# Performance work log

Hardware: AMD Instinct MI355X
Metric: run time of the kernel (lower is better)

Reference implementation:

```python
import jax, jax.numpy as jnp
import numpy as np

B, S, E, H = 2, 2048, 1024, 16
D = E // H  # head_dim = 64
SCALE = 1.0 / np.sqrt(D)


def setup_inputs() -> dict:
    key = jax.random.key(0)
    ks = jax.random.split(key, 5)
    std = 0.02
    return {
        "x": jax.random.normal(ks[0], (B, S, E), dtype=jnp.float32),
        "wq": jax.random.normal(ks[1], (E, E), dtype=jnp.float32) * std,
        "wk": jax.random.normal(ks[2], (E, E), dtype=jnp.float32) * std,
        "wv": jax.random.normal(ks[3], (E, E), dtype=jnp.float32) * std,
        "wo": jax.random.normal(ks[4], (E, E), dtype=jnp.float32) * std,
    }


def reference(x, wq, wk, wv, wo):
    # Linear projections (torch Linear: y = x @ W.T); weights stored as [out, in]
    q = jnp.einsum('bse,fe->bsf', x, wq)
    k = jnp.einsum('bse,fe->bsf', x, wk)
    v = jnp.einsum('bse,fe->bsf', x, wv)
    # split heads -> [B, H, S, D]
    q = q.reshape(B, S, H, D).transpose(0, 2, 1, 3)
    k = k.reshape(B, S, H, D).transpose(0, 2, 1, 3)
    v = v.reshape(B, S, H, D).transpose(0, 2, 1, 3)
    # scaled dot-product scores [B, H, S, S]
    scores = jnp.einsum('bhqd,bhkd->bhqk', q, k) * SCALE
    # causal mask: -inf above diagonal
    causal = jnp.triu(jnp.full((S, S), -jnp.inf, dtype=scores.dtype), k=1)
    scores = scores + causal[None, None, :, :]
    attn = jax.nn.softmax(scores, axis=-1)
    # dropout p=0 -> identity
    out = jnp.einsum('bhqk,bhkd->bhqd', attn, v)
    out = out.transpose(0, 2, 1, 3).reshape(B, S, E)
    return jnp.einsum('bse,fe->bsf', out, wo)
```

## Files before the change

### kernel.cpp

```cpp
#include <hip/hip_runtime.h>
#include <hip/hip_bf16.h>

#define B_ 2
#define S_ 2048
#define E_ 1024
#define H_ 16
#define D_ 64
#define QKV_N 3072
#define C2_ 0.18033688011112042f

typedef __attribute__((ext_vector_type(8))) unsigned short ushort8_t;
typedef __attribute__((ext_vector_type(8))) short short8_t;
typedef __attribute__((ext_vector_type(4))) float f32x4;

__device__ __forceinline__ unsigned short f2b(float f) {
    union { float f; unsigned u; } x; x.f = f;
    unsigned r = x.u + 0x7FFFu + ((x.u >> 16) & 1u);
    return (unsigned short)(r >> 16);
}
__device__ __forceinline__ ushort2 pkbf(float a, float b) {
    union { __hip_bfloat162 h; ushort2 u; } c;
    c.h = __float22bfloat162_rn(make_float2(a, b));
    return c.u;
}
__device__ __forceinline__ void glds16(const unsigned short* g, unsigned short* l) {
    __builtin_amdgcn_global_load_lds((const __attribute__((address_space(1))) void*)g,
                                     (__attribute__((address_space(3))) void*)l, 16, 0, 0);
}

__global__ __launch_bounds__(256) void cast_all(const float* __restrict__ x,
                                                const float* __restrict__ wq,
                                                const float* __restrict__ wk,
                                                const float* __restrict__ wv,
                                                const float* __restrict__ wo,
                                                unsigned short* __restrict__ xb,
                                                unsigned short* __restrict__ wb) {
    int idx = blockIdx.x * 256 + threadIdx.x;
    const float* src; unsigned short* dst; float s = 1.f; int j;
    if (idx < 1048576) {
        src = x; dst = xb; j = idx;
    } else {
        j = idx - 1048576;
        int y = j >> 18;
        src = (y == 0) ? wq : (y == 1) ? wk : (y == 2) ? wv : wo;
        dst = wb + (size_t)y * 1048576;
        j &= 262143;
        if (y == 0) s = C2_;
    }
    float4 v = ((const float4*)src)[j];
    ushort2 lo = pkbf(v.x * s, v.y * s), hi = pkbf(v.z * s, v.w * s);
    ((ushort4*)dst)[j] = make_ushort4(lo.x, lo.y, hi.x, hi.y);
}

template <int TM, bool OUT_BF16>
__device__ __forceinline__ void gemm_bt_body(const unsigned short* __restrict__ A,
                                             const unsigned short* __restrict__ Bt,
                                             void* __restrict__ Cout,
                                             int m0, int n0, int N, int K) {
    __shared__ unsigned short As[2 * TM * 32];
    __shared__ unsigned short Bs[2 * 128 * 32];
    const int tid = threadIdx.x;
    const int wave = tid >> 6;
    const int lane = tid & 63;
    const int wm = (wave >> 1) * (TM / 2);
    const int wn = (wave & 1) * 64;
    const int quad = lane >> 4;
    const int l15 = lane & 15;
    constexpr int MI = TM / 32;

    f32x4 acc[MI][4] = {};

    const int srow = lane >> 2;
    const int scb  = (lane & 3) * 8;
    const unsigned short* gB0 = Bt + (size_t)(n0 + wave * 32 + srow) * K + scb;
    const unsigned short* gB1 = gB0 + (size_t)16 * K;
    unsigned short* lB0 = Bs + wave * 1024;
    unsigned short* lB1 = lB0 + 512;
    const unsigned short* gA0;
    const unsigned short* gA1 = nullptr;
    unsigned short* lA0;
    unsigned short* lA1 = nullptr;
    if (TM == 128) {
        gA0 = A + (size_t)(m0 + wave * 32 + srow) * K + scb;
        gA1 = gA0 + (size_t)16 * K;
        lA0 = As + wave * 1024; lA1 = lA0 + 512;
    } else {
        gA0 = A + (size_t)(m0 + wave * 16 + srow) * K + scb;
        lA0 = As + wave * 512;
    }

    for (int k0 = 0; k0 < K; k0 += 64) {
        __syncthreads();
        glds16(gA0 + k0, lA0);
        glds16(gA0 + k0 + 32, lA0 + TM * 32);
        if (TM == 128) {
            glds16(gA1 + k0, lA1);
            glds16(gA1 + k0 + 32, lA1 + TM * 32);
        }
        glds16(gB0 + k0, lB0);
        glds16(gB0 + k0 + 32, lB0 + 128 * 32);
        glds16(gB1 + k0, lB1);
        glds16(gB1 + k0 + 32, lB1 + 128 * 32);
        __syncthreads();

#pragma unroll
        for (int h = 0; h < 2; ++h) {
            const unsigned short* ah = As + h * TM * 32;
            const unsigned short* bh = Bs + h * 128 * 32;
            short8_t af[MI], bfv[4];
#pragma unroll
            for (int mi = 0; mi < MI; ++mi)
                af[mi] = *(const short8_t*)(&ah[(wm + mi * 16 + l15) * 32 + quad * 8]);
#pragma unroll
            for (int ni = 0; ni < 4; ++ni)
                bfv[ni] = *(const short8_t*)(&bh[(wn + ni * 16 + l15) * 32 + quad * 8]);
#pragma unroll
            for (int mi = 0; mi < MI; ++mi)
#pragma unroll
                for (int ni = 0; ni < 4; ++ni)
                    acc[mi][ni] = __builtin_amdgcn_mfma_f32_16x16x32_bf16(
                        af[mi], bfv[ni], acc[mi][ni], 0, 0, 0);
        }
    }

#pragma unroll
    for (int mi = 0; mi < MI; ++mi)
#pragma unroll
        for (int ni = 0; ni < 4; ++ni)
#pragma unroll
            for (int r = 0; r < 4; ++r) {
                int row = m0 + wm + mi * 16 + quad * 4 + r;
                int col = n0 + wn + ni * 16 + l15;
                float val = acc[mi][ni][r];
                if (OUT_BF16)
                    ((unsigned short*)Cout)[(size_t)row * N + col] = f2b(val);
                else
                    ((float*)Cout)[(size_t)row * N + col] = val;
            }
}

__global__ __launch_bounds__(256, 3) void gemm_qkv(const unsigned short* __restrict__ xb,
                                                   const unsigned short* __restrict__ wqkv,
                                                   unsigned short* __restrict__ qkv) {
    int id = blockIdx.x + 24 * blockIdx.y;
    int sw = (id & 7) * 96 + (id >> 3);
    int n0 = (sw % 24) * 128;
    int m0 = (sw / 24) * 128;
    gemm_bt_body<128, true>(xb, wqkv, qkv, m0, n0, QKV_N, E_);
}

__global__ __launch_bounds__(256, 2) void gemm_out(const unsigned short* __restrict__ a,
                                                   const unsigned short* __restrict__ wob,
                                                   float* __restrict__ c) {
    gemm_bt_body<64, false>(a, wob, c, blockIdx.y * 64, blockIdx.x * 128, E_, E_);
}

__global__ __launch_bounds__(256) void transpose_v(const unsigned short* __restrict__ qkv,
                                                   unsigned short* __restrict__ Vt) {
    __shared__ unsigned short T[64][72];
    const int b = blockIdx.z, h = blockIdx.y, kt = blockIdx.x * 64;
    const int r = threadIdx.x >> 2;
    const int g = (threadIdx.x & 3) * 16;
    const size_t goff = (size_t)(b * S_ + kt + r) * QKV_N + 2048 + h * D_ + g;
    ushort8_t v0 = *(const ushort8_t*)(qkv + goff);
    ushort8_t v1 = *(const ushort8_t*)(qkv + goff + 8);
    *(ushort8_t*)(&T[r][g])     = v0;
    *(ushort8_t*)(&T[r][g + 8]) = v1;
    __syncthreads();
    ushort8_t o0, o1;
#pragma unroll
    for (int i = 0; i < 8; ++i) { o0[i] = T[g + i][r]; o1[i] = T[g + 8 + i][r]; }
    unsigned short* op = Vt + ((size_t)((b * H_ + h) * D_ + r)) * S_ + kt + g;
    *(ushort8_t*)(op)     = o0;
    *(ushort8_t*)(op + 8) = o1;
}

__global__ __launch_bounds__(512, 4) void attn_kernel(const unsigned short* __restrict__ QKV,
                                                      const unsigned short* __restrict__ Vtg,
                                                      unsigned short* __restrict__ O) {
    __shared__ unsigned short Ks[2][64 * 64];
    __shared__ unsigned short Vs[2][64 * 64];
    __shared__ unsigned short Ps[8][16 * 64];

    const int b = blockIdx.z, h = blockIdx.y;
    const int c = blockIdx.x;
    const int jp = (b == 0) ? c : (15 - c);
    const int tid = threadIdx.x;
    const int w = tid >> 6, lane = tid & 63;
    const int quad = lane >> 4, l15 = lane & 15;
    const int lx = l15 & 7;
    const int chunk = 2 * jp + ((w < 4) ? 1 : 0);
    const int Q0 = chunk * 64 + (w & 3) * 16;

    const size_t qo = (size_t)(b * S_ + Q0 + l15) * QKV_N + h * D_;
    short8_t bq0 = *(const short8_t*)(QKV + qo + quad * 8);
    short8_t bq1 = *(const short8_t*)(QKV + qo + 32 + quad * 8);

    f32x4 Oacc[4] = {};
    float lsum = 0.f;
    const int qg = Q0 + l15;

    const int fo0 = ((quad) ^ lx) * 8;
    const int fo1 = ((4 + quad) ^ lx) * 8;
    const int krow = l15 * 64;
    int pwo[4];
#pragma unroll
    for (int tm = 0; tm < 4; ++tm)
        pwo[tm] = ((tm * 2 + (quad >> 1)) ^ lx) * 8 + (quad & 1) * 4;

    const int srow = tid >> 3;
    const int scb  = tid & 7;
    const int swz  = (scb ^ (srow & 7)) * 8;
    const unsigned short* Kbase = QKV + (size_t)(b * S_) * QKV_N + 1024 + h * D_;
    const unsigned short* Vbase = Vtg + (size_t)((b * H_ + h) * D_) * S_;

    const int nT = jp + 1;
    for (int t = 0; t < nT; ++t) {
        const int kt0 = t * 128;
        ushort8_t ka = *(const ushort8_t*)(Kbase + (size_t)(kt0 + srow) * QKV_N + scb * 8);
        ushort8_t kb = *(const ushort8_t*)(Kbase + (size_t)(kt0 + 64 + srow) * QKV_N + scb * 8);
        ushort8_t va = *(const ushort8_t*)(Vbase + (size_t)srow * S_ + kt0 + scb * 8);
        ushort8_t vb = *(const ushort8_t*)(Vbase + (size_t)srow * S_ + kt0 + 64 + scb * 8);
        __syncthreads();
        *(ushort8_t*)(&Ks[0][srow * 64 + swz]) = ka;
        *(ushort8_t*)(&Ks[1][srow * 64 + swz]) = kb;
        *(ushort8_t*)(&Vs[0][srow * 64 + swz]) = va;
        *(ushort8_t*)(&Vs[1][srow * 64 + swz]) = vb;
        __syncthreads();

#pragma unroll
        for (int s = 0; s < 2; ++s) {
            const int kt = kt0 + s * 64;
            if (kt > Q0 + 15) continue;
            const bool h2 = (kt + 32 <= Q0 + 15);

            if (kt + 63 <= Q0) {
#pragma unroll
                for (int tm = 0; tm < 4; ++tm) {
                    short8_t ak0 = *(const short8_t*)(&Ks[s][tm * 1024 + krow + fo0]);
                    short8_t ak1 = *(const short8_t*)(&Ks[s][tm * 1024 + krow + fo1]);
                    f32x4 st = {0.f, 0.f, 0.f, 0.f};
                    st = __builtin_amdgcn_mfma_f32_16x16x32_bf16(ak0, bq0, st, 0, 0, 0);
                    st = __builtin_amdgcn_mfma_f32_16x16x32_bf16(ak1, bq1, st, 0, 0, 0);
                    float p0 = exp2f(st[0]), p1 = exp2f(st[1]);
                    float p2 = exp2f(st[2]), p3 = exp2f(st[3]);
                    lsum += (p0 + p1) + (p2 + p3);
                    ushort2 a = pkbf(p0, p1), c2 = pkbf(p2, p3);
                    *(ushort4*)(&Ps[w][krow + pwo[tm]]) = make_ushort4(a.x, a.y, c2.x, c2.y);
                }
            } else {
                const int need = h2 ? 4 : 2;
                for (int tm = 0; tm < need; ++tm) {
                    if (kt + tm * 16 <= Q0 + 15) {
                        short8_t ak0 = *(const short8_t*)(&Ks[s][tm * 1024 + krow + fo0]);
                        short8_t ak1 = *(const short8_t*)(&Ks[s][tm * 1024 + krow + fo1]);
                        f32x4 st = {0.f, 0.f, 0.f, 0.f};
                        st = __builtin_amdgcn_mfma_f32_16x16x32_bf16(ak0, bq0, st, 0, 0, 0);
                        st = __builtin_amdgcn_mfma_f32_16x16x32_bf16(ak1, bq1, st, 0, 0, 0);
                        const int kvb = kt + tm * 16 + quad * 4;
                        float p0 = (kvb     > qg) ? 0.f : exp2f(st[0]);
                        float p1 = (kvb + 1 > qg) ? 0.f : exp2f(st[1]);
                        float p2 = (kvb + 2 > qg) ? 0.f : exp2f(st[2]);
                        float p3 = (kvb + 3 > qg) ? 0.f : exp2f(st[3]);
                        lsum += (p0 + p1) + (p2 + p3);
                        ushort2 a = pkbf(p0, p1), c2 = pkbf(p2, p3);
                        *(ushort4*)(&Ps[w][krow + pwo[tm]]) = make_ushort4(a.x, a.y, c2.x, c2.y);
                    } else {
                        *(ushort4*)(&Ps[w][krow + pwo[tm]]) = make_ushort4(0, 0, 0, 0);
                    }
                }
            }

#pragma unroll
            for (int kh = 0; kh < 2; ++kh) {
                if (kh == 1 && !h2) break;
                const int fo = kh ? fo1 : fo0;
                short8_t bv[4];
#pragma unroll
                for (int tn = 0; tn < 4; ++tn)
                    bv[tn] = *(const short8_t*)(&Vs[s][tn * 1024 + krow + fo]);
                short8_t ap = *(const short8_t*)(&Ps[w][krow + fo]);
#pragma unroll
                for (int tn = 0; tn < 4; ++tn)
                    Oacc[tn] = __builtin_amdgcn_mfma_f32_16x16x32_bf16(
                        ap, bv[tn], Oacc[tn], 0, 0, 0);
            }
        }
    }

    float l = lsum;
    l += __shfl_xor(l, 16);
    l += __shfl_xor(l, 32);
    float inv = 1.f / l;
    float lir[4];
#pragma unroll
    for (int r = 0; r < 4; ++r)
        lir[r] = __shfl(inv, quad * 4 + r);
#pragma unroll
    for (int tn = 0; tn < 4; ++tn)
#pragma unroll
        for (int r = 0; r < 4; ++r) {
            int row = Q0 + quad * 4 + r;
            O[(size_t)(b * S_ + row) * E_ + h * D_ + tn * 16 + l15] =
                f2b(Oacc[tn][r] * lir[r]);
        }
}

extern "C" void kernel_launch(void* const* d_in, const int* in_sizes, int n_in,
                              void* d_out, int out_size, void* d_ws, size_t ws_size,
                              hipStream_t stream) {
    const float* x  = (const float*)d_in[0];
    const float* wq = (const float*)d_in[1];
    const float* wk = (const float*)d_in[2];
    const float* wv = (const float*)d_in[3];
    const float* wo = (const float*)d_in[4];
    float* out = (float*)d_out;

    unsigned short* ws   = (unsigned short*)d_ws;
    unsigned short* xb   = ws;
    unsigned short* wqkv = ws + 4194304;
    unsigned short* wob  = ws + 7340032;
    unsigned short* qkvb = ws + 8388608;
    unsigned short* ab   = ws + 20971520;
    unsigned short* vt   = xb;

    cast_all<<<8192, 256, 0, stream>>>(x, wq, wk, wv, wo, xb, wqkv);
    gemm_qkv<<<dim3(24, 32), 256, 0, stream>>>(xb, wqkv, qkvb);
    transpose_v<<<dim3(32, 16, 2), 256, 0, stream>>>(qkvb, vt);
    attn_kernel<<<dim3(16, 16, 2), 512, 0, stream>>>(qkvb, vt, ab);
    gemm_out<<<dim3(8, 64), 256, 0, stream>>>(ab, wob, out);
}
```

Baseline: 178.9 us.

## Fuse V transpose into QKV GEMM epilogue and rebalance causal chunk pairing

The QKV GEMM epilogue now writes V tiles transposed, packed into the V columns of the qkv buffer (two rows per head-dim channel). The attention kernel reads V^T directly from there, so the separate transpose_v launch and its extra global read/write pass go away. Attention work is also redistributed: each block now pairs query chunk c with chunk 31-c instead of the previous jp-based pairing. The trade-off is a more complex scattered epilogue store with 4-element ushort4 writes, and indexing that depends on the in-place layout being correct.

Measured after the change: 176.1 us. About the same (-1.6%).

```diff
diff --git a/kernel.cpp b/kernel.cpp
--- a/kernel.cpp
+++ b/kernel.cpp
@@ -52,7 +52,7 @@
     ((ushort4*)dst)[j] = make_ushort4(lo.x, lo.y, hi.x, hi.y);
 }
 
-template <int TM, bool OUT_BF16>
+template <int TM, bool OUT_BF16, bool VT>
 __device__ __forceinline__ void gemm_bt_body(const unsigned short* __restrict__ A,
                                              const unsigned short* __restrict__ Bt,
                                              void* __restrict__ Cout,
@@ -123,6 +123,22 @@
         }
     }
 
+    if (VT && n0 >= 2048) {
+#pragma unroll
+        for (int mi = 0; mi < MI; ++mi)
+#pragma unroll
+            for (int ni = 0; ni < 4; ++ni) {
+                int col = n0 + wn + ni * 16 + l15;
+                int r0  = m0 + wm + mi * 16 + quad * 4;
+                int bb  = r0 >> 11, s = r0 & 2047;
+                size_t drow = (size_t)bb * 2048 + 2 * (col - 2048) + (s >> 10);
+                unsigned short* dp = (unsigned short*)Cout + drow * QKV_N + 2048 + (s & 1023);
+                *(ushort4*)dp = make_ushort4(f2b(acc[mi][ni][0]), f2b(acc[mi][ni][1]),
+                                             f2b(acc[mi][ni][2]), f2b(acc[mi][ni][3]));
+            }
+        return;
+    }
+
 #pragma unroll
     for (int mi = 0; mi < MI; ++mi)
 #pragma unroll
@@ -146,37 +162,16 @@
     int sw = (id & 7) * 96 + (id >> 3);
     int n0 = (sw % 24) * 128;
     int m0 = (sw / 24) * 128;
-    gemm_bt_body<128, true>(xb, wqkv, qkv, m0, n0, QKV_N, E_);
+    gemm_bt_body<128, true, true>(xb, wqkv, qkv, m0, n0, QKV_N, E_);
 }
 
 __global__ __launch_bounds__(256, 2) void gemm_out(const unsigned short* __restrict__ a,
                                                    const unsigned short* __restrict__ wob,
                                                    float* __restrict__ c) {
-    gemm_bt_body<64, false>(a, wob, c, blockIdx.y * 64, blockIdx.x * 128, E_, E_);
-}
-
-__global__ __launch_bounds__(256) void transpose_v(const unsigned short* __restrict__ qkv,
-                                                   unsigned short* __restrict__ Vt) {
-    __shared__ unsigned short T[64][72];
-    const int b = blockIdx.z, h = blockIdx.y, kt = blockIdx.x * 64;
-    const int r = threadIdx.x >> 2;
-    const int g = (threadIdx.x & 3) * 16;
-    const size_t goff = (size_t)(b * S_ + kt + r) * QKV_N + 2048 + h * D_ + g;
-    ushort8_t v0 = *(const ushort8_t*)(qkv + goff);
-    ushort8_t v1 = *(const ushort8_t*)(qkv + goff + 8);
-    *(ushort8_t*)(&T[r][g])     = v0;
-    *(ushort8_t*)(&T[r][g + 8]) = v1;
-    __syncthreads();
-    ushort8_t o0, o1;
-#pragma unroll
-    for (int i = 0; i < 8; ++i) { o0[i] = T[g + i][r]; o1[i] = T[g + 8 + i][r]; }
-    unsigned short* op = Vt + ((size_t)((b * H_ + h) * D_ + r)) * S_ + kt + g;
-    *(ushort8_t*)(op)     = o0;
-    *(ushort8_t*)(op + 8) = o1;
+    gemm_bt_body<64, false, false>(a, wob, c, blockIdx.y * 64, blockIdx.x * 128, E_, E_);
 }
 
 __global__ __launch_bounds__(512, 4) void attn_kernel(const unsigned short* __restrict__ QKV,
-                                                      const unsigned short* __restrict__ Vtg,
                                                       unsigned short* __restrict__ O) {
     __shared__ unsigned short Ks[2][64 * 64];
     __shared__ unsigned short Vs[2][64 * 64];
@@ -184,12 +179,11 @@
 
     const int b = blockIdx.z, h = blockIdx.y;
     const int c = blockIdx.x;
-    const int jp = (b == 0) ? c : (15 - c);
     const int tid = threadIdx.x;
     const int w = tid >> 6, lane = tid & 63;
     const int quad = lane >> 4, l15 = lane & 15;
     const int lx = l15 & 7;
-    const int chunk = 2 * jp + ((w < 4) ? 1 : 0);
+    const int chunk = (w < 4) ? (31 - c) : c;
     const int Q0 = chunk * 64 + (w & 3) * 16;
 
     const size_t qo = (size_t)(b * S_ + Q0 + l15) * QKV_N + h * D_;
@@ -212,15 +206,18 @@
     const int scb  = tid & 7;
     const int swz  = (scb ^ (srow & 7)) * 8;
     const unsigned short* Kbase = QKV + (size_t)(b * S_) * QKV_N + 1024 + h * D_;
-    const unsigned short* Vbase = Vtg + (size_t)((b * H_ + h) * D_) * S_;
-
-    const int nT = jp + 1;
+    const unsigned short* Vb2 = QKV + (size_t)(b * S_ + 2 * (h * D_ + srow)) * QKV_N + 2048;
+
+    const int ntiles = 32 - c;
+    const int nT = (ntiles + 1) >> 1;
     for (int t = 0; t < nT; ++t) {
         const int kt0 = t * 128;
         ushort8_t ka = *(const ushort8_t*)(Kbase + (size_t)(kt0 + srow) * QKV_N + scb * 8);
         ushort8_t kb = *(const ushort8_t*)(Kbase + (size_t)(kt0 + 64 + srow) * QKV_N + scb * 8);
-        ushort8_t va = *(const ushort8_t*)(Vbase + (size_t)srow * S_ + kt0 + scb * 8);
-        ushort8_t vb = *(const ushort8_t*)(Vbase + (size_t)srow * S_ + kt0 + 64 + scb * 8);
+        ushort8_t va = *(const ushort8_t*)(Vb2 + (size_t)(kt0 >> 10) * QKV_N
+                                               + (kt0 & 1023) + scb * 8);
+        ushort8_t vb = *(const ushort8_t*)(Vb2 + (size_t)((kt0 + 64) >> 10) * QKV_N
+                                               + ((kt0 + 64) & 1023) + scb * 8);
         __syncthreads();
         *(ushort8_t*)(&Ks[0][srow * 64 + swz]) = ka;
         *(ushort8_t*)(&Ks[1][srow * 64 + swz]) = kb;
@@ -322,11 +319,9 @@
     unsigned short* wob  = ws + 7340032;
     unsigned short* qkvb = ws + 8388608;
     unsigned short* ab   = ws + 20971520;
-    unsigned short* vt   = xb;
 
     cast_all<<<8192, 256, 0, stream>>>(x, wq, wk, wv, wo, xb, wqkv);
     gemm_qkv<<<dim3(24, 32), 256, 0, stream>>>(xb, wqkv, qkvb);
-    transpose_v<<<dim3(32, 16, 2), 256, 0, stream>>>(qkvb, vt);
-    attn_kernel<<<dim3(16, 16, 2), 512, 0, stream>>>(qkvb, vt, ab);
+    attn_kernel<<<dim3(16, 16, 2), 512, 0, stream>>>(qkvb, ab);
     gemm_out<<<dim3(8, 64), 256, 0, stream>>>(ab, wob, out);
 }
```
